# Kernel tuning notes

Measured on AMD Instinct MI355X. Metric: run time of the kernel, lower is better.

## Reference

```python
import jax, jax.numpy as jnp
import numpy as np

B, T, K, V, D, C = 16, 16, 4, 10003, 256, 64  # batch, traj_len, beam, lid_size+3, dim_embed_loc, dim_com


def setup_inputs() -> dict:
    key = jax.random.key(0)
    ks = jax.random.split(key, 9)
    return {
        "loc_tar": jax.random.randint(ks[0], (B, T), 0, V),
        "zs": jax.random.normal(ks[1], (B, D), jnp.float32),
        "zt": jax.random.normal(ks[2], (B, D), jnp.float32),
        "E": jax.random.normal(ks[3], (V, D), jnp.float32) * 0.02,    # loc embedding table
        "W_v": jax.random.normal(ks[4], (D, V), jnp.float32) * 0.02,  # decoder output proj
        "b_v": jnp.zeros((V,), jnp.float32),
        "W_c": jax.random.normal(ks[5], (D, C), jnp.float32) * 0.05,  # LocCompressor
        "b_c": jnp.zeros((C,), jnp.float32),
        "W_t": jax.random.normal(ks[6], (C,), jnp.float32) * 0.05,    # temporal decoder
        "W_zt": jax.random.normal(ks[7], (D,), jnp.float32) * 0.05,
    }


def _decode(loc_tar, zs, E, W_v, b_v):
    # Beam-search decode faithful to the torch inference branch:
    # per-step full-seq decoder fwd, log_softmax, topk, (log-prob) product,
    # descending sort over M*K candidates, gather top 2K chains.
    chain_r = loc_tar.at[:, 1:].set(0)   # [B,T]; keep BOS, zero rest
    zs_r = zs                            # [B,D]
    prob = None
    for i in range(T - 1):
        emb = E[chain_r]                                     # [N,T,D] gather
        h = emb + zs_r[:, None, :]
        logp = jax.nn.log_softmax(h @ W_v + b_v, axis=-1)    # [N,T,V]
        p_i, idx_i = jax.lax.top_k(logp[:, i, :], K)         # [N,K]
        if i == 0:
            chain_r = jnp.repeat(chain_r, K, axis=0).at[:, 1].set(idx_i.reshape(-1))  # [B*K,T]
            prob = p_i                                       # [B,K]
            zs_r = jnp.repeat(zs_r, K, axis=0)
        else:
            M = chain_r.shape[0] // B                        # K at i=1, 2K after
            # NOTE: original multiplies log-probs (faithful to source)
            prob2 = (prob[:, :, None] * p_i.reshape(B, M, K)).reshape(B, M * K)
            order = jnp.argsort(-prob2, axis=-1)             # descending sort
            prob = jnp.take_along_axis(prob2, order, axis=-1)[:, :2 * K]
            ch = jnp.repeat(chain_r, K, axis=0).at[:, i + 1].set(idx_i.reshape(-1))
            ch = ch.reshape(B, M * K, T)
            chain_r = ch[jnp.arange(B)[:, None], order[:, :2 * K]].reshape(-1, T)  # [B*2K,T]
            zs_r = jnp.repeat(zs, 2 * K, axis=0)
    return chain_r.reshape(B, -1, T)[:, 0, 1:-1]             # best beam, [B,T-2]


def reference(loc_tar, zs, zt, E, W_v, b_v, W_c, b_c, W_t, W_zt):
    loc_chain = _decode(loc_tar, zs, E, W_v, b_v)            # [B,T-2] int
    loc_info = jnp.tanh(E[loc_chain] @ W_c + b_c)            # LocCompressor, [B,T-2,C]
    tim_chain = loc_info @ W_t + (zt @ W_zt)[:, None]        # temporal decoder, [B,T-2]
    return loc_chain, tim_chain
```

## Files before the change

kernel.cpp:

```cpp
#include <hip/hip_runtime.h>
#include <math.h>

#define BB 16
#define TT 16
#define KK 4
#define VV 10003
#define DD 256
#define CC 64
#define RPB 4
#define VT  1280
#define NVT 8
#define VP 10016
#define FNEG (-1e30f)

typedef float f32x4 __attribute__((ext_vector_type(4)));
typedef float f32x4u __attribute__((ext_vector_type(4), aligned(4)));

struct L4 { float v0, v1, v2, v3; int i0, i1, i2, i3; };

__device__ __forceinline__ void l4_init(L4 &l) {
  l.v0 = l.v1 = l.v2 = l.v3 = FNEG;
  l.i0 = l.i1 = l.i2 = l.i3 = 0x7fffffff;
}
__device__ __forceinline__ bool better(float v, int ix, float v2, int ix2) {
  return (v > v2) || (v == v2 && ix < ix2);
}
__device__ __forceinline__ void l4_insert(L4 &l, float v, int ix) {
  const bool c0 = better(v, ix, l.v0, l.i0);
  const bool c1 = better(v, ix, l.v1, l.i1);
  const bool c2 = better(v, ix, l.v2, l.i2);
  const bool c3 = better(v, ix, l.v3, l.i3);
  l.v3 = c3 ? (c2 ? l.v2 : v) : l.v3;  l.i3 = c3 ? (c2 ? l.i2 : ix) : l.i3;
  l.v2 = c2 ? (c1 ? l.v1 : v) : l.v2;  l.i2 = c2 ? (c1 ? l.i1 : ix) : l.i2;
  l.v1 = c1 ? (c0 ? l.v0 : v) : l.v1;  l.i1 = c1 ? (c0 ? l.i0 : ix) : l.i1;
  l.v0 = c0 ? v : l.v0;                l.i0 = c0 ? ix : l.i0;
}
__device__ __forceinline__ void l4_merge(L4 &a, const L4 &b) {
  l4_insert(a, b.v0, b.i0);
  l4_insert(a, b.v1, b.i1);
  l4_insert(a, b.v2, b.i2);
  l4_insert(a, b.v3, b.i3);
}
__device__ __forceinline__ L4 l4_shfl_xor(const L4 &a, int off) {
  L4 o;
  o.v0 = __shfl_xor(a.v0, off); o.i0 = __shfl_xor(a.i0, off);
  o.v1 = __shfl_xor(a.v1, off); o.i1 = __shfl_xor(a.i1, off);
  o.v2 = __shfl_xor(a.v2, off); o.i2 = __shfl_xor(a.i2, off);
  o.v3 = __shfl_xor(a.v3, off); o.i3 = __shfl_xor(a.i3, off);
  return o;
}

__device__ float np_block_sum(const float* a, int n) {
  float r0=a[0],r1=a[1],r2=a[2],r3=a[3],r4=a[4],r5=a[5],r6=a[6],r7=a[7];
  int i;
  for (i = 8; i + 8 <= n; i += 8) {
    r0 += a[i+0]; r1 += a[i+1]; r2 += a[i+2]; r3 += a[i+3];
    r4 += a[i+4]; r5 += a[i+5]; r6 += a[i+6]; r7 += a[i+7];
  }
  float res = ((r0 + r1) + (r2 + r3)) + ((r4 + r5) + (r6 + r7));
  for (; i < n; ++i) res += a[i];
  return res;
}

__global__ void k_init(const int* __restrict__ loc_tar, int* __restrict__ chainA) {
  int t = threadIdx.x;
  int b = t >> 4, j = t & 15;
  chainA[t] = (j == 0) ? loc_tar[b * TT] : 0;
}

__global__ __launch_bounds__(256, 1)
void k_gemm(const float* __restrict__ E, const float* __restrict__ zs,
            const float* __restrict__ Wv, const float* __restrict__ bv,
            const int* __restrict__ chain, float* __restrict__ Lg,
            int step, int N, int Mshift) {
  __shared__ __align__(16) float xs[RPB * DD];
  __shared__ int cs[RPB];

  const int t = threadIdx.x;
  const int tile = blockIdx.x % NVT;
  const int n0 = (blockIdx.x / NVT) * RPB;
  const int v0 = tile * VT;

  const int v4 = v0 + (t << 2);
  const int v1 = v0 + 1024 + t;
  const int v1ok = (v1 < VV);
  const int v1c = v1ok ? v1 : (VV - 1);

  if (t < RPB) {
    int n = n0 + t;
    int c = chain[n * TT + step];
    if ((unsigned)c >= VV) c = 0;
    cs[t] = c;
  }
  __syncthreads();

  for (int e = t; e < RPB * DD; e += 256) {
    int r = e >> 8, d = e & 255;
    int n = n0 + r;
    int b = n >> Mshift;
    xs[e] = E[cs[r] * DD + d] + zs[b * DD + d];
  }
  __syncthreads();

  const float* w4p = Wv + v4;
  const float* w1p = Wv + v1c;

  float acc4[RPB][4];
  float acc1[RPB];
#pragma unroll
  for (int r = 0; r < RPB; ++r) {
    acc1[r] = 0.f;
#pragma unroll
    for (int j = 0; j < 4; ++j) acc4[r][j] = 0.f;
  }

  f32x4u w4A[8], w4B[8];
  float  w1A[8], w1B[8];
  f32x4  h0A[RPB], h1A[RPB], h0B[RPB], h1B[RPB];

#pragma unroll
  for (int u = 0; u < 8; ++u) {
    w4A[u] = *(const f32x4u*)(w4p + (size_t)u * VV);
    w1A[u] = w1p[(size_t)u * VV];
  }
#pragma unroll
  for (int r = 0; r < RPB; ++r) {
    h0A[r] = *(const f32x4*)(xs + r * DD);
    h1A[r] = *(const f32x4*)(xs + r * DD + 4);
  }

  for (int d0 = 0; d0 < DD; d0 += 16) {
    const int dB = d0 + 8;
#pragma unroll
    for (int u = 0; u < 8; ++u) {
      w4B[u] = *(const f32x4u*)(w4p + (size_t)(dB + u) * VV);
      w1B[u] = w1p[(size_t)(dB + u) * VV];
    }
#pragma unroll
    for (int r = 0; r < RPB; ++r) {
      h0B[r] = *(const f32x4*)(xs + r * DD + dB);
      h1B[r] = *(const f32x4*)(xs + r * DD + dB + 4);
    }

#pragma unroll
    for (int u = 0; u < 8; ++u) {
#pragma unroll
      for (int r = 0; r < RPB; ++r) {
        const float hv = (u < 4) ? h0A[r][u] : h1A[r][u - 4];
#pragma unroll
        for (int j = 0; j < 4; ++j) acc4[r][j] = fmaf(hv, w4A[u][j], acc4[r][j]);
        acc1[r] = fmaf(hv, w1A[u], acc1[r]);
      }
    }

    const int dA = (d0 + 16 < DD) ? (d0 + 16) : 0;
#pragma unroll
    for (int u = 0; u < 8; ++u) {
      w4A[u] = *(const f32x4u*)(w4p + (size_t)(dA + u) * VV);
      w1A[u] = w1p[(size_t)(dA + u) * VV];
    }
#pragma unroll
    for (int r = 0; r < RPB; ++r) {
      h0A[r] = *(const f32x4*)(xs + r * DD + dA);
      h1A[r] = *(const f32x4*)(xs + r * DD + dA + 4);
    }

#pragma unroll
    for (int u = 0; u < 8; ++u) {
#pragma unroll
      for (int r = 0; r < RPB; ++r) {
        const float hv = (u < 4) ? h0B[r][u] : h1B[r][u - 4];
#pragma unroll
        for (int j = 0; j < 4; ++j) acc4[r][j] = fmaf(hv, w4B[u][j], acc4[r][j]);
        acc1[r] = fmaf(hv, w1B[u], acc1[r]);
      }
    }
  }

  const f32x4u bv4 = *(const f32x4u*)(bv + v4);
#pragma unroll
  for (int r = 0; r < RPB; ++r) {
    f32x4 o;
#pragma unroll
    for (int j = 0; j < 4; ++j) o[j] = acc4[r][j] + bv4[j];
    *(f32x4*)(Lg + (size_t)(n0 + r) * VP + v4) = o;
  }
  if (v1ok) {
    const float bvv = bv[v1];
#pragma unroll
    for (int r = 0; r < RPB; ++r)
      Lg[(size_t)(n0 + r) * VP + v1] = acc1[r] + bvv;
  }
}

__global__ __launch_bounds__(1024)
void k_red(const float* __restrict__ Lg, float* __restrict__ topP,
           int* __restrict__ topI) {
  __shared__ __align__(16) float row[VV];
  __shared__ int   segBase[255];
  __shared__ int   segN[255];
  __shared__ float val[255];
  __shared__ float wmax[16];
  __shared__ float wv4[16 * 4];
  __shared__ int   wi4[16 * 4];
  __shared__ float gmS;
  __shared__ float gtv[4];
  __shared__ int   gti[4];

  const int n = blockIdx.x;
  const int t = threadIdx.x;
  const int lane = t & 63;
  const int wid = t >> 6;
  const float* grow = Lg + (size_t)n * VP;

  const int va = t << 2;
  const int vb = 4096 + (t << 2);
  const int vc = 8192 + (t << 2);
  f32x4 xa = *(const f32x4*)(grow + va);
  f32x4 xb = *(const f32x4*)(grow + vb);
  f32x4 xc;
  const bool cfull = (vc + 3 < VV);
  if (cfull) {
    xc = *(const f32x4*)(grow + vc);
  } else {
#pragma unroll
    for (int j = 0; j < 4; ++j) xc[j] = (vc + j < VV) ? grow[vc + j] : FNEG;
  }

  float m = FNEG;
  L4 top; l4_init(top);
#pragma unroll
  for (int j = 0; j < 4; ++j) { float x = xa[j]; if (x > m) m = x; l4_insert(top, x, va + j); }
#pragma unroll
  for (int j = 0; j < 4; ++j) { float x = xb[j]; if (x > m) m = x; l4_insert(top, x, vb + j); }
#pragma unroll
  for (int j = 0; j < 4; ++j) {
    if (vc + j < VV) { float x = xc[j]; if (x > m) m = x; l4_insert(top, x, vc + j); }
  }

  for (int off = 32; off; off >>= 1) {
    float m2 = __shfl_xor(m, off);
    if (m2 > m) m = m2;
    L4 o = l4_shfl_xor(top, off);
    l4_merge(top, o);
  }
  if (lane == 0) {
    wmax[wid] = m;
    wv4[wid * 4 + 0] = top.v0; wi4[wid * 4 + 0] = top.i0;
    wv4[wid * 4 + 1] = top.v1; wi4[wid * 4 + 1] = top.i1;
    wv4[wid * 4 + 2] = top.v2; wi4[wid * 4 + 2] = top.i2;
    wv4[wid * 4 + 3] = top.v3; wi4[wid * 4 + 3] = top.i3;
  }
  if (t == 0) { segBase[0] = 0; segN[0] = VV; }
  __syncthreads();

  if (t < 16) {
    float mm = wmax[t];
    L4 a;
    a.v0 = wv4[t * 4 + 0]; a.i0 = wi4[t * 4 + 0];
    a.v1 = wv4[t * 4 + 1]; a.i1 = wi4[t * 4 + 1];
    a.v2 = wv4[t * 4 + 2]; a.i2 = wi4[t * 4 + 2];
    a.v3 = wv4[t * 4 + 3]; a.i3 = wi4[t * 4 + 3];
    for (int off = 1; off < 16; off <<= 1) {
      float m2 = __shfl_xor(mm, off);
      if (m2 > mm) mm = m2;
      L4 o = l4_shfl_xor(a, off);
      l4_merge(a, o);
    }
    if (t == 0) {
      gmS = mm;
      gtv[0] = a.v0; gti[0] = a.i0;
      gtv[1] = a.v1; gti[1] = a.i1;
      gtv[2] = a.v2; gti[2] = a.i2;
      gtv[3] = a.v3; gti[3] = a.i3;
    }
  }

  for (int L = 0; L < 7; ++L) {
    int first = (1 << L) - 1, cnt = 1 << L;
    if (t < cnt) {
      int p = first + t;
      int np_ = segN[p], bp = segBase[p];
      int n2 = np_ / 2; n2 -= n2 % 8;
      segBase[2 * p + 1] = bp;       segN[2 * p + 1] = n2;
      segBase[2 * p + 2] = bp + n2;  segN[2 * p + 2] = np_ - n2;
    }
    __syncthreads();
  }
  const float gm = gmS;

  {
    f32x4 ea, eb;
#pragma unroll
    for (int j = 0; j < 4; ++j) ea[j] = (float)exp((double)(xa[j] - gm));
#pragma unroll
    for (int j = 0; j < 4; ++j) eb[j] = (float)exp((double)(xb[j] - gm));
    *(f32x4*)(row + va) = ea;
    *(f32x4*)(row + vb) = eb;
    if (cfull) {
      f32x4 ec;
#pragma unroll
      for (int j = 0; j < 4; ++j) ec[j] = (float)exp((double)(xc[j] - gm));
      *(f32x4*)(row + vc) = ec;
    } else {
#pragma unroll
      for (int j = 0; j < 4; ++j)
        if (vc + j < VV) row[vc + j] = (float)exp((double)(xc[j] - gm));
    }
  }
  __syncthreads();

  if (t < 128) {
    int nd = 127 + t;
    val[nd] = np_block_sum(&row[segBase[nd]], segN[nd]);
  }
  for (int L = 6; L >= 0; --L) {
    __syncthreads();
    int first = (1 << L) - 1, cnt = 1 << L;
    if (t < cnt) {
      int p = first + t;
      val[p] = val[2 * p + 1] + val[2 * p + 2];
    }
  }

  if (t == 0) {
    float ls = (float)log((double)val[0]);
#pragma unroll
    for (int j = 0; j < 4; ++j) {
      topP[n * 4 + j] = (gtv[j] - gm) - ls;
      topI[n * 4 + j] = gti[j];
    }
  }
}

__global__ __launch_bounds__(512)
void k_beam(const float* __restrict__ topP, const int* __restrict__ topI,
            float* __restrict__ prob, const int* __restrict__ chain_cur,
            int* __restrict__ chain_next, int step) {
  __shared__ int sel_src[BB][8];
  __shared__ int sel_tok[BB][8];

  const int tid = threadIdx.x;
  const int b = tid >> 5;
  const int c = tid & 31;

  if (step == 0) {
    for (int e = tid; e < BB * KK * TT; e += 512) {
      int dst = e >> 4, q = e & 15;
      int bb = dst >> 2, kk = dst & 3;
      int val;
      if (q == 1) {
        int tok = topI[bb * 4 + kk]; if ((unsigned)tok >= VV) tok = 0;
        val = tok;
      } else {
        val = chain_cur[bb * TT + q];
      }
      chain_next[dst * TT + q] = val;
    }
    if (tid < BB * KK) {
      int bb = tid >> 2, kk = tid & 3;
      prob[bb * 8 + kk] = topP[bb * 4 + kk];
    }
    return;
  }

  const int M = (step == 1) ? 4 : 8;
  const int nc = M * 4;

  float act;
  if (c < nc) {
    int m = c >> 2, k = c & 3;
    act = prob[b * 8 + m] * topP[(b * M + m) * 4 + k];
  } else {
    act = -INFINITY;
  }

  for (int j = 0; j < 8; ++j) {
    float rv = act; int ri = c;
#pragma unroll
    for (int off = 1; off < 32; off <<= 1) {
      float v2 = __shfl_xor(rv, off, 32);
      int   i2 = __shfl_xor(ri, off, 32);
      if (v2 > rv || (v2 == rv && i2 < ri)) { rv = v2; ri = i2; }
    }
    if (c == ri) act = -INFINITY;
    if (c == 0) {
      int m = ri >> 2, k = ri & 3;
      int src = b * M + m;
      int tok = topI[src * 4 + k]; if ((unsigned)tok >= VV) tok = 0;
      sel_src[b][j] = src;
      sel_tok[b][j] = tok;
      prob[b * 8 + j] = rv;
    }
  }
  __syncthreads();

  for (int e = tid; e < BB * 8 * TT; e += 512) {
    int dst = e >> 4, q = e & 15;
    int bb = dst >> 3, j = dst & 7;
    int src = sel_src[bb][j];
    int val = (q == step + 1) ? sel_tok[bb][j] : chain_cur[src * TT + q];
    chain_next[dst * TT + q] = val;
  }
}

__global__ __launch_bounds__(64)
void k_final(const int* __restrict__ chain, const float* __restrict__ E,
             const float* __restrict__ Wc, const float* __restrict__ bc,
             const float* __restrict__ Wt, const float* __restrict__ zt,
             const float* __restrict__ Wzt, float* __restrict__ out) {
  int blk = blockIdx.x;
  int b = blk / (TT - 2), t = blk % (TT - 2);
  int lane = threadIdx.x;
  int loc = chain[(b * 8) * TT + 1 + t];
  if ((unsigned)loc >= VV) loc = 0;
  double acc = (double)bc[lane];
  const float* er = E + loc * DD;
  for (int d = 0; d < DD; ++d) acc += (double)er[d] * (double)Wc[d * CC + lane];
  double val = tanh(acc) * (double)Wt[lane];
  const float* ztr = zt + b * DD;
#pragma unroll
  for (int q = 0; q < 4; ++q) val += (double)ztr[lane * 4 + q] * (double)Wzt[lane * 4 + q];
  for (int off = 32; off; off >>= 1) val += __shfl_down(val, off);
  if (lane == 0) {
    out[b * (TT - 2) + t] = (float)loc;
    out[BB * (TT - 2) + b * (TT - 2) + t] = (float)val;
  }
}

extern "C" void kernel_launch(void* const* d_in, const int* in_sizes, int n_in,
                              void* d_out, int out_size, void* d_ws, size_t ws_size,
                              hipStream_t stream) {
  const int*   loc_tar = (const int*)  d_in[0];
  const float* zs      = (const float*)d_in[1];
  const float* zt      = (const float*)d_in[2];
  const float* E       = (const float*)d_in[3];
  const float* Wv      = (const float*)d_in[4];
  const float* bv      = (const float*)d_in[5];
  const float* Wc      = (const float*)d_in[6];
  const float* bc      = (const float*)d_in[7];
  const float* Wt      = (const float*)d_in[8];
  const float* Wzt     = (const float*)d_in[9];
  float* out = (float*)d_out;

  char* w = (char*)d_ws;
  float* Lg     = (float*)(w);
  float* topP   = (float*)(w + 5128192);
  int*   topI   = (int*)  (w + 5130240);
  float* prob   = (float*)(w + 5132288);
  int*   chainA = (int*)  (w + 5132800);
  int*   chainB = (int*)  (w + 5140992);

  k_init<<<1, 256, 0, stream>>>(loc_tar, chainA);

  int N = BB;
  int* cur = chainA;
  int* nxt = chainB;
  for (int i = 0; i < TT - 1; ++i) {
    int Mshift = (i == 0) ? 0 : ((i == 1) ? 2 : 3);
    int nrg = N / RPB;
    k_gemm<<<nrg * NVT, 256, 0, stream>>>(E, zs, Wv, bv, cur, Lg, i, N, Mshift);
    k_red<<<N, 1024, 0, stream>>>(Lg, topP, topI);
    k_beam<<<1, 512, 0, stream>>>(topP, topI, prob, cur, nxt, i);
    int* t2 = cur; cur = nxt; nxt = t2;
    N = (i == 0) ? BB * KK : BB * 2 * KK;
  }

  k_final<<<BB * (TT - 2), 64, 0, stream>>>(cur, E, Wc, bc, Wt, zt, Wzt, out);
}
```

Measured before the change: 1.043 ms.

## Fuse beam selection into reduction kernel via last-block atomic ticket

```diff
diff --git a/kernel.cpp b/kernel.cpp
--- a/kernel.cpp
+++ b/kernel.cpp
@@ -62,10 +62,12 @@
   return res;
 }
 
-__global__ void k_init(const int* __restrict__ loc_tar, int* __restrict__ chainA) {
+__global__ void k_init(const int* __restrict__ loc_tar, int* __restrict__ chainA,
+                       int* __restrict__ bar) {
   int t = threadIdx.x;
   int b = t >> 4, j = t & 15;
   chainA[t] = (j == 0) ? loc_tar[b * TT] : 0;
+  if (t == 0) bar[0] = 0;
 }
 
 __global__ __launch_bounds__(256, 1)
@@ -195,17 +197,16 @@
 
 __global__ __launch_bounds__(1024)
 void k_red(const float* __restrict__ Lg, float* __restrict__ topP,
-           int* __restrict__ topI) {
+           int* __restrict__ topI, float* __restrict__ prob,
+           const int* __restrict__ chain_cur, int* __restrict__ chain_next,
+           int step, int* __restrict__ bar) {
   __shared__ __align__(16) float row[VV];
-  __shared__ int   segBase[255];
-  __shared__ int   segN[255];
-  __shared__ float val[255];
   __shared__ float wmax[16];
   __shared__ float wv4[16 * 4];
   __shared__ int   wi4[16 * 4];
-  __shared__ float gmS;
-  __shared__ float gtv[4];
-  __shared__ int   gti[4];
+  __shared__ int   lastF;
+  __shared__ int   sel_src[BB][8];
+  __shared__ int   sel_tok[BB][8];
 
   const int n = blockIdx.x;
   const int t = threadIdx.x;
@@ -251,43 +252,29 @@
     wv4[wid * 4 + 2] = top.v2; wi4[wid * 4 + 2] = top.i2;
     wv4[wid * 4 + 3] = top.v3; wi4[wid * 4 + 3] = top.i3;
   }
-  if (t == 0) { segBase[0] = 0; segN[0] = VV; }
-  __syncthreads();
-
-  if (t < 16) {
-    float mm = wmax[t];
-    L4 a;
-    a.v0 = wv4[t * 4 + 0]; a.i0 = wi4[t * 4 + 0];
-    a.v1 = wv4[t * 4 + 1]; a.i1 = wi4[t * 4 + 1];
-    a.v2 = wv4[t * 4 + 2]; a.i2 = wi4[t * 4 + 2];
-    a.v3 = wv4[t * 4 + 3]; a.i3 = wi4[t * 4 + 3];
-    for (int off = 1; off < 16; off <<= 1) {
-      float m2 = __shfl_xor(mm, off);
-      if (m2 > mm) mm = m2;
-      L4 o = l4_shfl_xor(a, off);
-      l4_merge(a, o);
-    }
-    if (t == 0) {
-      gmS = mm;
-      gtv[0] = a.v0; gti[0] = a.i0;
-      gtv[1] = a.v1; gti[1] = a.i1;
-      gtv[2] = a.v2; gti[2] = a.i2;
-      gtv[3] = a.v3; gti[3] = a.i3;
-    }
-  }
-
-  for (int L = 0; L < 7; ++L) {
-    int first = (1 << L) - 1, cnt = 1 << L;
-    if (t < cnt) {
-      int p = first + t;
-      int np_ = segN[p], bp = segBase[p];
-      int n2 = np_ / 2; n2 -= n2 % 8;
-      segBase[2 * p + 1] = bp;       segN[2 * p + 1] = n2;
-      segBase[2 * p + 2] = bp + n2;  segN[2 * p + 2] = np_ - n2;
-    }
-    __syncthreads();
-  }
-  const float gm = gmS;
+  __syncthreads();
+
+  float mm = wmax[lane & 15];
+#pragma unroll
+  for (int off = 8; off; off >>= 1) {
+    float m2 = __shfl_xor(mm, off);
+    if (m2 > mm) mm = m2;
+  }
+  const float gm = mm;
+
+  L4 aa; l4_init(aa);
+  if (wid == 0) {
+    const int g = lane & 15;
+    aa.v0 = wv4[g * 4 + 0]; aa.i0 = wi4[g * 4 + 0];
+    aa.v1 = wv4[g * 4 + 1]; aa.i1 = wi4[g * 4 + 1];
+    aa.v2 = wv4[g * 4 + 2]; aa.i2 = wi4[g * 4 + 2];
+    aa.v3 = wv4[g * 4 + 3]; aa.i3 = wi4[g * 4 + 3];
+#pragma unroll
+    for (int off = 8; off; off >>= 1) {
+      L4 o = l4_shfl_xor(aa, off);
+      l4_merge(aa, o);
+    }
+  }
 
   {
     f32x4 ea, eb;
@@ -310,42 +297,47 @@
   }
   __syncthreads();
 
-  if (t < 128) {
-    int nd = 127 + t;
-    val[nd] = np_block_sum(&row[segBase[nd]], segN[nd]);
-  }
-  for (int L = 6; L >= 0; --L) {
-    __syncthreads();
-    int first = (1 << L) - 1, cnt = 1 << L;
-    if (t < cnt) {
-      int p = first + t;
-      val[p] = val[2 * p + 1] + val[2 * p + 2];
-    }
+  float rootv = 0.f;
+  if (t < 64) {
+    int base = 0, nn = VV;
+#pragma unroll
+    for (int k = 5; k >= 0; --k) {
+      int half = nn >> 1;
+      int n2 = half - (half & 7);
+      if ((t >> k) & 1) { base += n2; nn -= n2; } else nn = n2;
+    }
+    int half = nn >> 1;
+    int n2 = half - (half & 7);
+    float sa = np_block_sum(&row[base], n2);
+    float sb = np_block_sum(&row[base + n2], nn - n2);
+    float v = sa + sb;
+#pragma unroll
+    for (int l = 0; l < 6; ++l) {
+      float x0 = __shfl(v, t * 2);
+      float x1 = __shfl(v, t * 2 + 1);
+      v = x0 + x1;
+    }
+    rootv = v;
   }
 
   if (t == 0) {
-    float ls = (float)log((double)val[0]);
-#pragma unroll
-    for (int j = 0; j < 4; ++j) {
-      topP[n * 4 + j] = (gtv[j] - gm) - ls;
-      topI[n * 4 + j] = gti[j];
-    }
-  }
-}
-
-__global__ __launch_bounds__(512)
-void k_beam(const float* __restrict__ topP, const int* __restrict__ topI,
-            float* __restrict__ prob, const int* __restrict__ chain_cur,
-            int* __restrict__ chain_next, int step) {
-  __shared__ int sel_src[BB][8];
-  __shared__ int sel_tok[BB][8];
-
-  const int tid = threadIdx.x;
-  const int b = tid >> 5;
-  const int c = tid & 31;
+    float ls = (float)log((double)rootv);
+    topP[n * 4 + 0] = (aa.v0 - gm) - ls;  topI[n * 4 + 0] = aa.i0;
+    topP[n * 4 + 1] = (aa.v1 - gm) - ls;  topI[n * 4 + 1] = aa.i1;
+    topP[n * 4 + 2] = (aa.v2 - gm) - ls;  topI[n * 4 + 2] = aa.i2;
+    topP[n * 4 + 3] = (aa.v3 - gm) - ls;  topI[n * 4 + 3] = aa.i3;
+    __threadfence();
+    int ticket = atomicAdd(bar, 1);
+    lastF = (ticket == (int)gridDim.x - 1);
+  }
+  __syncthreads();
+  if (!lastF) return;
+
+  __threadfence();
+  if (t == 0) *bar = 0;
 
   if (step == 0) {
-    for (int e = tid; e < BB * KK * TT; e += 512) {
+    for (int e = t; e < BB * KK * TT; e += 1024) {
       int dst = e >> 4, q = e & 15;
       int bb = dst >> 2, kk = dst & 3;
       int val;
@@ -357,8 +349,8 @@
       }
       chain_next[dst * TT + q] = val;
     }
-    if (tid < BB * KK) {
-      int bb = tid >> 2, kk = tid & 3;
+    if (t < BB * KK) {
+      int bb = t >> 2, kk = t & 3;
       prob[bb * 8 + kk] = topP[bb * 4 + kk];
     }
     return;
@@ -367,35 +359,38 @@
   const int M = (step == 1) ? 4 : 8;
   const int nc = M * 4;
 
-  float act;
-  if (c < nc) {
-    int m = c >> 2, k = c & 3;
-    act = prob[b * 8 + m] * topP[(b * M + m) * 4 + k];
-  } else {
-    act = -INFINITY;
-  }
-
-  for (int j = 0; j < 8; ++j) {
-    float rv = act; int ri = c;
-#pragma unroll
-    for (int off = 1; off < 32; off <<= 1) {
-      float v2 = __shfl_xor(rv, off, 32);
-      int   i2 = __shfl_xor(ri, off, 32);
-      if (v2 > rv || (v2 == rv && i2 < ri)) { rv = v2; ri = i2; }
-    }
-    if (c == ri) act = -INFINITY;
-    if (c == 0) {
-      int m = ri >> 2, k = ri & 3;
-      int src = b * M + m;
-      int tok = topI[src * 4 + k]; if ((unsigned)tok >= VV) tok = 0;
-      sel_src[b][j] = src;
-      sel_tok[b][j] = tok;
-      prob[b * 8 + j] = rv;
-    }
-  }
-  __syncthreads();
-
-  for (int e = tid; e < BB * 8 * TT; e += 512) {
+  if (t < 512) {
+    const int b = t >> 5;
+    const int c = t & 31;
+    float act;
+    if (c < nc) {
+      int mi = c >> 2, k = c & 3;
+      act = prob[b * 8 + mi] * topP[(b * M + mi) * 4 + k];
+    } else {
+      act = -INFINITY;
+    }
+    for (int j = 0; j < 8; ++j) {
+      float rv = act; int ri = c;
+#pragma unroll
+      for (int off = 1; off < 32; off <<= 1) {
+        float v2 = __shfl_xor(rv, off, 32);
+        int   i2 = __shfl_xor(ri, off, 32);
+        if (v2 > rv || (v2 == rv && i2 < ri)) { rv = v2; ri = i2; }
+      }
+      if (c == ri) act = -INFINITY;
+      if (c == 0) {
+        int mi = ri >> 2, k = ri & 3;
+        int src = b * M + mi;
+        int tok = topI[src * 4 + k]; if ((unsigned)tok >= VV) tok = 0;
+        sel_src[b][j] = src;
+        sel_tok[b][j] = tok;
+        prob[b * 8 + j] = rv;
+      }
+    }
+  }
+  __syncthreads();
+
+  for (int e = t; e < BB * 8 * TT; e += 1024) {
     int dst = e >> 4, q = e & 15;
     int bb = dst >> 3, j = dst & 7;
     int src = sel_src[bb][j];
@@ -450,8 +445,9 @@
   float* prob   = (float*)(w + 5132288);
   int*   chainA = (int*)  (w + 5132800);
   int*   chainB = (int*)  (w + 5140992);
-
-  k_init<<<1, 256, 0, stream>>>(loc_tar, chainA);
+  int*   bar    = (int*)  (w + 5149184);
+
+  k_init<<<1, 256, 0, stream>>>(loc_tar, chainA, bar);
 
   int N = BB;
   int* cur = chainA;
@@ -460,8 +456,7 @@
     int Mshift = (i == 0) ? 0 : ((i == 1) ? 2 : 3);
     int nrg = N / RPB;
     k_gemm<<<nrg * NVT, 256, 0, stream>>>(E, zs, Wv, bv, cur, Lg, i, N, Mshift);
-    k_red<<<N, 1024, 0, stream>>>(Lg, topP, topI);
-    k_beam<<<1, 512, 0, stream>>>(topP, topI, prob, cur, nxt, i);
+    k_red<<<N, 1024, 0, stream>>>(Lg, topP, topI, prob, cur, nxt, i, bar);
     int* t2 = cur; cur = nxt; nxt = t2;
     N = (i == 0) ? BB * KK : BB * 2 * KK;
   }
```

After: 1.077 ms. 1.03x slower.
